# Kernel optimization log

Hardware: AMD Instinct MI355X
Metric: run time of the kernel (lower is better)

## Reference

```python
import jax, jax.numpy as jnp
import numpy as np

L, D, H, V, BS = 12, 768, 12, 50257, 1024  # n_layer, n_embd, n_head, vocab, block_size
B, T = 2, 1024
HD = D // H
SCALE = HD ** -0.5


def setup_inputs() -> dict:
    key = jax.random.key(0)
    ks = jax.random.split(key, 10)
    s = 0.02  # init std from _init_weights
    f = lambda k, shape: jax.random.normal(k, shape, jnp.float32) * s
    return {
        "idx": jax.random.randint(ks[0], (B, T), 0, V),
        "tok_emb": f(ks[1], (V, D)),          # tied with LM head
        "pos_emb": f(ks[2], (BS, D)),
        "wqkv": f(ks[3], (L, 3 * D, D)), "bqkv": jnp.zeros((L, 3 * D), jnp.float32),
        "wproj": f(ks[4], (L, D, D)),    "bproj": jnp.zeros((L, D), jnp.float32),
        "ln1_g": jnp.ones((L, D), jnp.float32), "ln1_b": jnp.zeros((L, D), jnp.float32),
        "ln2_g": jnp.ones((L, D), jnp.float32), "ln2_b": jnp.zeros((L, D), jnp.float32),
        "w1": f(ks[5], (L, 4 * D, D)), "b1": jnp.zeros((L, 4 * D), jnp.float32),
        "w2": f(ks[6], (L, D, 4 * D)), "b2": jnp.zeros((L, D), jnp.float32),
        "lnf_g": jnp.ones((D,), jnp.float32), "lnf_b": jnp.zeros((D,), jnp.float32),
    }


def _ln(x, g, b, eps=1e-5):
    mu = jnp.mean(x, axis=-1, keepdims=True)
    var = jnp.mean(jnp.square(x - mu), axis=-1, keepdims=True)
    return (x - mu) * jax.lax.rsqrt(var + eps) * g + b


def _gpt_forward(idx, tok_emb, pos_emb, wqkv, bqkv, wproj, bproj,
                 ln1_g, ln1_b, ln2_g, ln2_b, w1, b1, w2, b2, lnf_g, lnf_b):
    Bb, Tt = idx.shape
    x = tok_emb[idx] + pos_emb[:Tt]  # [B,T,D]; dropout=0 in eval
    causal = jnp.tril(jnp.ones((Tt, Tt), bool))

    def block(x, p):
        wq, bq, wp, bp, g1, be1, g2, be2, W1, B1, W2, B2 = p
        h = _ln(x, g1, be1)
        qkv = h @ wq.T + bq                       # [B,T,3D]
        q, k, v = jnp.split(qkv, 3, axis=-1)
        to_heads = lambda z: z.reshape(Bb, Tt, H, HD).transpose(0, 2, 1, 3)
        q, k, v = to_heads(q), to_heads(k), to_heads(v)
        att = jnp.einsum('bhqd,bhkd->bhqk', q, k) * SCALE
        att = jnp.where(causal, att, -jnp.inf)
        att = jax.nn.softmax(att, axis=-1)
        y = jnp.einsum('bhqk,bhkd->bhqd', att, v)
        y = y.transpose(0, 2, 1, 3).reshape(Bb, Tt, D)
        x = x + (y @ wp.T + bp)
        h2 = _ln(x, g2, be2)
        ff = jax.nn.gelu(h2 @ W1.T + B1, approximate=False) @ W2.T + B2
        return x + ff, None

    layer_params = (wqkv, bqkv, wproj, bproj, ln1_g, ln1_b, ln2_g, ln2_b, w1, b1, w2, b2)
    x, _ = jax.lax.scan(block, x, layer_params)
    x = _ln(x, lnf_g, lnf_b)
    return x @ tok_emb.T  # tied LM head, [B,T,V]


def reference(idx, tok_emb, pos_emb, wqkv, bqkv, wproj, bproj,
              ln1_g, ln1_b, ln2_g, ln2_b, w1, b1, w2, b2, lnf_g, lnf_b):
    return _gpt_forward(idx, tok_emb, pos_emb, wqkv, bqkv, wproj, bproj,
                        ln1_g, ln1_b, ln2_g, ln2_b, w1, b1, w2, b2, lnf_g, lnf_b)
```

## Files before the change

kernel.cpp:

```cpp
#include <hip/hip_runtime.h>
#include <hip/hip_bf16.h>
#include <type_traits>

#define TT 1024
#define DD 768
#define HH 12
#define LL 12
#define VV 50257
#define MROWS 2048

typedef __attribute__((ext_vector_type(4))) float f32x4;
typedef __attribute__((ext_vector_type(16))) float f32x16;
typedef __attribute__((ext_vector_type(8))) short bf16x8;

__device__ __forceinline__ short f2bf(float f) {
  __hip_bfloat16 h = __float2bfloat16(f);
  short s;
  __builtin_memcpy(&s, &h, 2);
  return s;
}

__device__ __forceinline__ void gload16(const void* g, void* l) {
  __builtin_amdgcn_global_load_lds(
      (const __attribute__((address_space(1))) unsigned int*)g,
      (__attribute__((address_space(3))) unsigned int*)l, 16, 0, 0);
}

__device__ __forceinline__ float wsum(float v) {
#pragma unroll
  for (int o = 32; o; o >>= 1) v += __shfl_xor(v, o, 64);
  return v;
}

struct CvtArgs { const float* s[5]; short* d[5]; long n4[5]; };

__global__ __launch_bounds__(256) void cvt5_k(CvtArgs a, long tot)
{
  const long stride = (long)gridDim.x * 256;
  for (long i = (long)blockIdx.x * 256 + threadIdx.x; i < tot; i += stride) {
    long off = i;
    int s = 0;
#pragma unroll
    for (int q = 0; q < 4; ++q) {
      if (off >= a.n4[s]) { off -= a.n4[s]; ++s; }
    }
    const float4 v = ((const float4*)a.s[s])[off];
    short4 h;
    h.x = f2bf(v.x); h.y = f2bf(v.y); h.z = f2bf(v.z); h.w = f2bf(v.w);
    ((short4*)a.d[s])[off] = h;
  }
}

__global__ __launch_bounds__(256) void embed_k(const int* __restrict__ idx,
    const float* __restrict__ tok, const float* __restrict__ pos,
    float* __restrict__ x)
{
  int i = blockIdx.x * 256 + threadIdx.x;
  int d = i % DD;
  int bt = i / DD;
  int t = bt & (TT - 1);
  x[i] = tok[(long)idx[bt] * DD + d] + pos[t * DD + d];
}

__global__ __launch_bounds__(256) void ln_k(const float* __restrict__ x,
    const float* __restrict__ g, const float* __restrict__ b,
    short* __restrict__ out)
{
  const int w = threadIdx.x >> 6;
  const int lane = threadIdx.x & 63;
  const int row = blockIdx.x * 4 + w;
  const float* xr = x + (long)row * DD;
  float4 v[3];
  float s = 0.f, s2 = 0.f;
#pragma unroll
  for (int i = 0; i < 3; ++i) {
    v[i] = ((const float4*)xr)[lane + i * 64];
    s  += v[i].x + v[i].y + v[i].z + v[i].w;
    s2 += v[i].x * v[i].x + v[i].y * v[i].y + v[i].z * v[i].z + v[i].w * v[i].w;
  }
  s = wsum(s); s2 = wsum(s2);
  const float mu = s * (1.f / DD);
  const float var = s2 * (1.f / DD) - mu * mu;
  const float rstd = rsqrtf(var + 1e-5f);
#pragma unroll
  for (int i = 0; i < 3; ++i) {
    const int d0 = (lane + i * 64) * 4;
    short4 h;
    h.x = f2bf((v[i].x - mu) * rstd * g[d0 + 0] + b[d0 + 0]);
    h.y = f2bf((v[i].y - mu) * rstd * g[d0 + 1] + b[d0 + 1]);
    h.z = f2bf((v[i].z - mu) * rstd * g[d0 + 2] + b[d0 + 2]);
    h.w = f2bf((v[i].w - mu) * rstd * g[d0 + 3] + b[d0 + 3]);
    ((short4*)(out + (long)row * DD))[lane + i * 64] = h;
  }
}

__global__ __launch_bounds__(256) void flash_k(const short* __restrict__ qkv,
                                               const short* __restrict__ vt,
                                               short* __restrict__ y)
{
  const int qt = (int)gridDim.x - 1 - (int)blockIdx.x;
  const int z  = blockIdx.y;
  const int zb = z / HH, zh = z % HH;
  const int w    = threadIdx.x >> 6;
  const int lane = threadIdx.x & 63;
  const int c = lane & 15, g = lane >> 4;

  __shared__ __align__(16) short Pl[4][16][72];
  __shared__ float Ol[4][16][64];
  __shared__ float ml[4][16], ll[4][16];

  const int qbase = qt * 16;
  const long rowQ = (long)(zb * TT + qbase + c) * (3 * DD) + zh * 64;

  bf16x8 qf[2];
  qf[0] = *(const bf16x8*)(qkv + rowQ + g * 8);
  qf[1] = *(const bf16x8*)(qkv + rowQ + 32 + g * 8);

  f32x4 O[4] = {};
  f32x4 mrun, lrun;
#pragma unroll
  for (int r = 0; r < 4; ++r) { mrun[r] = -1e30f; lrun[r] = 0.f; }

  const float CSC = 0.125f * 1.44269504089f;
  const int nt = (qbase + 15) / 64 + 1;

  for (int t = w; t < nt; t += 4) {
    const int k0 = t * 64;
    f32x4 acc[4] = {};
#pragma unroll
    for (int nf = 0; nf < 4; ++nf) {
      const long rowK = (long)(zb * TT + k0 + nf * 16 + c) * (3 * DD) + DD + zh * 64;
      bf16x8 kf0 = *(const bf16x8*)(qkv + rowK + g * 8);
      bf16x8 kf1 = *(const bf16x8*)(qkv + rowK + 32 + g * 8);
      acc[nf] = __builtin_amdgcn_mfma_f32_16x16x32_bf16(qf[0], kf0, acc[nf], 0, 0, 0);
      acc[nf] = __builtin_amdgcn_mfma_f32_16x16x32_bf16(qf[1], kf1, acc[nf], 0, 0, 0);
    }
    f32x4 tv[4];
    const int mask_needed = (k0 + 63 > qbase);
#pragma unroll
    for (int nf = 0; nf < 4; ++nf) {
      const int k_abs = k0 + nf * 16 + c;
#pragma unroll
      for (int r = 0; r < 4; ++r) {
        float val = acc[nf][r] * CSC;
        if (mask_needed && k_abs > qbase + g * 4 + r) val = -1e30f;
        tv[nf][r] = val;
      }
    }
    f32x4 rmax;
#pragma unroll
    for (int r = 0; r < 4; ++r)
      rmax[r] = fmaxf(fmaxf(tv[0][r], tv[1][r]), fmaxf(tv[2][r], tv[3][r]));
#pragma unroll
    for (int off = 1; off < 16; off <<= 1) {
#pragma unroll
      for (int r = 0; r < 4; ++r) rmax[r] = fmaxf(rmax[r], __shfl_xor(rmax[r], off, 64));
    }
    f32x4 mnew, rfac;
#pragma unroll
    for (int r = 0; r < 4; ++r) {
      mnew[r] = fmaxf(mrun[r], rmax[r]);
      rfac[r] = exp2f(mrun[r] - mnew[r]);
      mrun[r] = mnew[r];
    }
    f32x4 e[4], rsum;
#pragma unroll
    for (int r = 0; r < 4; ++r) rsum[r] = 0.f;
#pragma unroll
    for (int nf = 0; nf < 4; ++nf)
#pragma unroll
      for (int r = 0; r < 4; ++r) {
        e[nf][r] = exp2f(tv[nf][r] - mnew[r]);
        rsum[r] += e[nf][r];
      }
#pragma unroll
    for (int off = 1; off < 16; off <<= 1) {
#pragma unroll
      for (int r = 0; r < 4; ++r) rsum[r] += __shfl_xor(rsum[r], off, 64);
    }
#pragma unroll
    for (int r = 0; r < 4; ++r) lrun[r] = lrun[r] * rfac[r] + rsum[r];
#pragma unroll
    for (int nf = 0; nf < 4; ++nf)
#pragma unroll
      for (int r = 0; r < 4; ++r) O[nf][r] *= rfac[r];
#pragma unroll
    for (int nf = 0; nf < 4; ++nf)
#pragma unroll
      for (int r = 0; r < 4; ++r)
        Pl[w][g * 4 + r][nf * 16 + c] = f2bf(e[nf][r]);
    asm volatile("s_waitcnt lgkmcnt(0)" ::: "memory");
    bf16x8 pf[2];
    pf[0] = *(const bf16x8*)&Pl[w][c][g * 8];
    pf[1] = *(const bf16x8*)&Pl[w][c][32 + g * 8];
#pragma unroll
    for (int nf = 0; nf < 4; ++nf) {
      const long vrow = ((long)z * 64 + nf * 16 + c) * TT + k0;
      const bf16x8 vf0 = *(const bf16x8*)(vt + vrow + g * 8);
      const bf16x8 vf1 = *(const bf16x8*)(vt + vrow + 32 + g * 8);
      O[nf] = __builtin_amdgcn_mfma_f32_16x16x32_bf16(pf[0], vf0, O[nf], 0, 0, 0);
      O[nf] = __builtin_amdgcn_mfma_f32_16x16x32_bf16(pf[1], vf1, O[nf], 0, 0, 0);
    }
  }

#pragma unroll
  for (int nf = 0; nf < 4; ++nf)
#pragma unroll
    for (int r = 0; r < 4; ++r)
      Ol[w][g * 4 + r][nf * 16 + c] = O[nf][r];
  if (c == 0) {
#pragma unroll
    for (int r = 0; r < 4; ++r) { ml[w][g * 4 + r] = mrun[r]; ll[w][g * 4 + r] = lrun[r]; }
  }
  __syncthreads();

  for (int e2 = threadIdx.x; e2 < 16 * 64; e2 += 256) {
    const int row = e2 >> 6, d = e2 & 63;
    const float M = fmaxf(fmaxf(ml[0][row], ml[1][row]), fmaxf(ml[2][row], ml[3][row]));
    float L = 0.f, Ov = 0.f;
#pragma unroll
    for (int u = 0; u < 4; ++u) {
      const float f = exp2f(ml[u][row] - M);
      L += ll[u][row] * f;
      Ov += Ol[u][row][d] * f;
    }
    y[(long)(zb * TT + qbase + row) * DD + zh * 64 + d] = f2bf(Ov / L);
  }
}

template<int BM, int BN, int BK, int MFS, typename TB, int EPI, bool LMSWZ, bool PIPE>
__global__ __launch_bounds__(256) void gemm_nt(
    const short* __restrict__ A, const TB* __restrict__ Bm,
    const float* __restrict__ bias, const float* __restrict__ resid,
    void* __restrict__ Cout,
    int M, int N, int K, int lda, int ldb, int ldc,
    long aSB, long aSH, long bSB, long bSH, long cSB, long cSH,
    float scale, int causal)
{
  int n0, m0;
  if constexpr (LMSWZ) {
    const int l = blockIdx.x;
    const int x = l & 7;
    const int j = l >> 3;
    const int mt = j & 15;
    const int nl = j >> 4;
    const int npan = (N + BN - 1) / BN;
    const int q = npan >> 3, rr = npan & 7;
    const int cnt = q + (x < rr);
    if (nl >= cnt) return;
    const int nstart = x * q + (x < rr ? x : rr);
    n0 = (nstart + nl) * BN;
    m0 = mt * BM;
  } else {
    n0 = blockIdx.x * BN;
    m0 = blockIdx.y * BM;
  }
  if (causal && n0 >= m0 + BM) return;
  const int z = blockIdx.z;
  const int zb = z / HH, zh = z % HH;
  const short* Ag = A + zb * aSB + zh * aSH + (long)m0 * lda;
  const TB*    Bg = Bm + zb * bSB + zh * bSH;
  const long  cOff = zb * cSB + zh * cSH;

  constexpr int NBUF = PIPE ? 2 : 1;
  __shared__ __align__(16) short Als[NBUF][BM][BK];
  __shared__ __align__(16) short Bls[NBUF][BN][BK];

  const int tid = threadIdx.x;
  const int lane = tid & 63, wid = tid >> 6;
  constexpr int WTM = BM / 2, WTN = BN / 2;
  constexpr int FM = WTM / 16, FN = WTN / 16;
  constexpr int FM2 = (MFS == 32) ? WTM / 32 : 1;
  constexpr int FN2 = (MFS == 32) ? WTN / 32 : 1;
  constexpr int AM = (MFS == 16) ? FM : FM2;
  constexpr int AN = (MFS == 16) ? FN : FN2;
  const int wr = wid >> 1, wc = wid & 1;

  using accT = typename std::conditional<MFS == 16, f32x4, f32x16>::type;
  accT acc[AM][AN] = {};

  constexpr bool B_IS_F32 = (sizeof(TB) == 4);
  constexpr int CPR = BK / 8;
  constexpr int NCA = BM * CPR;
  constexpr int NCB = BN * CPR;
  constexpr int IA = NCA / 256, IB = NCB / 256;
  constexpr int GPT = IA + IB;
  static_assert(CPR == 8, "swizzle assumes 128B rows (BK=64)");
  static_assert(B_IS_F32 || (NCA % 256 == 0 && NCB % 256 == 0), "chunk grid");

  auto compute = [&](int buf) {
    if constexpr (MFS == 16) {
      const int kAoff = (lane >> 4) * 8;
#pragma unroll
      for (int kk = 0; kk < BK; kk += 32) {
        bf16x8 af[AM], bfr[AN];
#pragma unroll
        for (int mi = 0; mi < AM; ++mi) {
          const int Ra = wr * WTM + mi * 16 + (lane & 15);
          const int kca = (kk + kAoff) >> 3;
          af[mi] = *(const bf16x8*)&Als[buf][Ra][(kca ^ (Ra & 7)) << 3];
        }
#pragma unroll
        for (int ni = 0; ni < AN; ++ni) {
          const int Rb = wc * WTN + ni * 16 + (lane & 15);
          const int kcb = (kk + kAoff) >> 3;
          bfr[ni] = *(const bf16x8*)&Bls[buf][Rb][(kcb ^ (Rb & 7)) << 3];
        }
#pragma unroll
        for (int mi = 0; mi < AM; ++mi)
#pragma unroll
          for (int ni = 0; ni < AN; ++ni)
            acc[mi][ni] = __builtin_amdgcn_mfma_f32_16x16x32_bf16(af[mi], bfr[ni], acc[mi][ni], 0, 0, 0);
      }
    } else {
#pragma unroll
      for (int kk = 0; kk < BK; kk += 16) {
        const int kc = (kk >> 3) + (lane >> 5);
        bf16x8 af[AM], bfr[AN];
#pragma unroll
        for (int mi = 0; mi < AM; ++mi) {
          const int Ra = wr * WTM + mi * 32 + (lane & 31);
          af[mi] = *(const bf16x8*)&Als[buf][Ra][(kc ^ (Ra & 7)) << 3];
        }
#pragma unroll
        for (int ni = 0; ni < AN; ++ni) {
          const int Rb = wc * WTN + ni * 32 + (lane & 31);
          bfr[ni] = *(const bf16x8*)&Bls[buf][Rb][(kc ^ (Rb & 7)) << 3];
        }
#pragma unroll
        for (int mi = 0; mi < AM; ++mi)
#pragma unroll
          for (int ni = 0; ni < AN; ++ni)
            acc[mi][ni] = __builtin_amdgcn_mfma_f32_32x32x16_bf16(af[mi], bfr[ni], acc[mi][ni], 0, 0, 0);
      }
    }
  };

  if constexpr (!B_IS_F32) {
    const short* ap[IA];
    const short* bp[IB];
#pragma unroll
    for (int i = 0; i < IA; ++i) {
      const int cch = i * 256 + tid;
      const int r = cch / CPR, kc = cch % CPR;
      ap[i] = Ag + (long)r * lda + ((kc ^ (r & 7)) << 3);
    }
#pragma unroll
    for (int i = 0; i < IB; ++i) {
      const int cch = i * 256 + tid;
      const int r = cch / CPR, kc = cch % CPR;
      int gr = n0 + r; gr = (gr < N) ? gr : (N - 1);
      bp[i] = (const short*)Bg + (long)gr * ldb + ((kc ^ (r & 7)) << 3);
    }
    const int ldsoff = wid * 64 * 16;

    auto stage = [&](int buf) {
#pragma unroll
      for (int i = 0; i < IA; ++i) {
        gload16(ap[i], (char*)&Als[buf][0][0] + i * 4096 + ldsoff);
        ap[i] += BK;
      }
#pragma unroll
      for (int i = 0; i < IB; ++i) {
        gload16(bp[i], (char*)&Bls[buf][0][0] + i * 4096 + ldsoff);
        bp[i] += BK;
      }
    };

    if constexpr (PIPE) {
      const int KT = K / BK;
      stage(0);
      for (int kt = 0; kt < KT; ++kt) {
        const int cur = kt & 1;
        if (kt + 1 < KT) {
          stage(cur ^ 1);
          asm volatile("s_waitcnt vmcnt(%0)" :: "i"(GPT));
        } else {
          asm volatile("s_waitcnt vmcnt(0)");
        }
        __builtin_amdgcn_sched_barrier(0);
        __builtin_amdgcn_s_barrier();
        __builtin_amdgcn_sched_barrier(0);
        compute(cur);
        asm volatile("" ::: "memory");
        __builtin_amdgcn_s_barrier();
        __builtin_amdgcn_sched_barrier(0);
      }
    } else {
      const int KT = K / BK;
      for (int kt = 0; kt < KT; ++kt) {
        stage(0);
        __syncthreads();
        compute(0);
        __syncthreads();
      }
    }
  } else {
    for (int k0 = 0; k0 < K; k0 += BK) {
#pragma unroll
      for (int cc = tid; cc < BM * (BK / 8); cc += 256) {
        int r = cc / (BK / 8), kc = cc % (BK / 8);
        const uint4 v = *(const uint4*)(Ag + (long)r * lda + k0 + kc * 8);
        *(uint4*)((char*)&Als[0][r][0] + ((kc ^ (r & 7)) << 4)) = v;
      }
#pragma unroll
      for (int cc = tid; cc < BN * (BK / 4); cc += 256) {
        int r = cc / (BK / 4), kc = cc % (BK / 4);
        int gr = n0 + r; gr = (gr < N) ? gr : (N - 1);
        const float4 v = *(const float4*)((const float*)Bg + (long)gr * ldb + k0 + kc * 4);
        short4 h4;
        h4.x = f2bf(v.x); h4.y = f2bf(v.y); h4.z = f2bf(v.z); h4.w = f2bf(v.w);
        *(short4*)((char*)&Bls[0][r][0] + ((kc * 8) ^ ((r & 7) << 4))) = h4;
      }
      __syncthreads();
      compute(0);
      __syncthreads();
    }
  }

  if constexpr (MFS == 16) {
    const int rq = (lane >> 4) << 2;
    const int cl = lane & 15;
#pragma unroll
    for (int mi = 0; mi < AM; ++mi) {
#pragma unroll
      for (int ni = 0; ni < AN; ++ni) {
        const int cg = n0 + wc * WTN + ni * 16 + cl;
        if (cg >= N) continue;
        const int rbase = m0 + wr * WTM + mi * 16 + rq;
        if constexpr (EPI == 5) {
          if (cg >= 2 * DD) {
            const int hh = (cg - 2 * DD) >> 6, dd2 = (cg - 2 * DD) & 63;
            const int bI = rbase >> 10, tI = rbase & (TT - 1);
            const float bv = bias[cg];
            short4 h4;
            h4.x = f2bf(acc[mi][ni][0] + bv);
            h4.y = f2bf(acc[mi][ni][1] + bv);
            h4.z = f2bf(acc[mi][ni][2] + bv);
            h4.w = f2bf(acc[mi][ni][3] + bv);
            short* vtp = (short*)(void*)resid;
            *(short4*)(vtp + (((long)(bI * HH + hh) * 64 + dd2) << 10) + tI) = h4;
          } else {
#pragma unroll
            for (int q = 0; q < 4; ++q)
              ((short*)Cout)[(long)(rbase + q) * ldc + cg] = f2bf(acc[mi][ni][q] + bias[cg]);
          }
          continue;
        }
#pragma unroll
        for (int q = 0; q < 4; ++q) {
          const long cidx = cOff + (long)(rbase + q) * ldc + cg;
          const float v = acc[mi][ni][q];
          if constexpr (EPI == 0) {
            ((float*)Cout)[cidx] = v * scale;
          } else if constexpr (EPI == 1) {
            ((short*)Cout)[cidx] = f2bf(v + bias[cg]);
          } else if constexpr (EPI == 2) {
            ((float*)Cout)[cidx] = resid[cidx] + v + bias[cg];
          } else if constexpr (EPI == 3) {
            const float zz = v + bias[cg];
            ((short*)Cout)[cidx] = f2bf(0.5f * zz * (1.f + erff(zz * 0.70710678118f)));
          } else {
            ((short*)Cout)[cidx] = f2bf(v);
          }
        }
      }
    }
  } else {
    const int cl = lane & 31;
    const int rhi = (lane >> 5) * 4;
#pragma unroll
    for (int mi = 0; mi < AM; ++mi) {
#pragma unroll
      for (int ni = 0; ni < AN; ++ni) {
        const int cg = n0 + wc * WTN + ni * 32 + cl;
        if (cg >= N) continue;
#pragma unroll
        for (int reg = 0; reg < 16; ++reg) {
          const int row = m0 + wr * WTM + mi * 32 + (reg & 3) + ((reg >> 2) * 8) + rhi;
          const long cidx = cOff + (long)row * ldc + cg;
          const float v = acc[mi][ni][reg];
          if constexpr (EPI == 0) {
            ((float*)Cout)[cidx] = v * scale;
          } else if constexpr (EPI == 1) {
            ((short*)Cout)[cidx] = f2bf(v + bias[cg]);
          } else if constexpr (EPI == 2) {
            ((float*)Cout)[cidx] = resid[cidx] + v + bias[cg];
          } else if constexpr (EPI == 3) {
            const float zz = v + bias[cg];
            ((short*)Cout)[cidx] = f2bf(0.5f * zz * (1.f + erff(zz * 0.70710678118f)));
          } else {
            ((short*)Cout)[cidx] = f2bf(v);
          }
        }
      }
    }
  }
}

template<typename TB>
static void run_model(const int* idx, const float* tok_f, const float* pos,
                      const TB* wqkv, const float* bqkv, const TB* wproj, const float* bproj,
                      const float* ln1g, const float* ln1b, const float* ln2g, const float* ln2b,
                      const TB* w1, const float* b1, const TB* w2, const float* b2,
                      const float* lnfg, const float* lnfb, const TB* tok_w,
                      float* xa, float* xb, short* hbf, short* qkv, short* vt,
                      short* ybf, short* ffb,
                      float* out, hipStream_t stream)
{
  embed_k<<<dim3(MROWS * DD / 256), 256, 0, stream>>>(idx, tok_f, pos, xa);

  float* xc = xa;
  float* xn = xb;
  for (int l = 0; l < LL; ++l) {
    ln_k<<<dim3(MROWS / 4), 256, 0, stream>>>(xc, ln1g + l * DD, ln1b + l * DD, hbf);
    gemm_nt<128, 64, 64, 16, TB, 5, false, true><<<dim3(36, 16, 1), 256, 0, stream>>>(
        hbf, wqkv + (long)l * 3 * DD * DD, bqkv + l * 3 * DD, (const float*)vt, qkv,
        MROWS, 3 * DD, DD, DD, DD, 3 * DD, 0, 0, 0, 0, 0, 0, 1.f, 0);
    flash_k<<<dim3(64, 24), 256, 0, stream>>>(qkv, vt, ybf);
    gemm_nt<64, 64, 64, 16, TB, 2, false, true><<<dim3(12, 32, 1), 256, 0, stream>>>(
        ybf, wproj + (long)l * DD * DD, bproj + l * DD, xc, xn,
        MROWS, DD, DD, DD, DD, DD, 0, 0, 0, 0, 0, 0, 1.f, 0);
    ln_k<<<dim3(MROWS / 4), 256, 0, stream>>>(xn, ln2g + l * DD, ln2b + l * DD, hbf);
    gemm_nt<128, 64, 64, 16, TB, 3, false, true><<<dim3(48, 16, 1), 256, 0, stream>>>(
        hbf, w1 + (long)l * 4 * DD * DD, b1 + l * 4 * DD, nullptr, ffb,
        MROWS, 4 * DD, DD, DD, DD, 4 * DD, 0, 0, 0, 0, 0, 0, 1.f, 0);
    gemm_nt<64, 64, 64, 16, TB, 2, false, true><<<dim3(12, 32, 1), 256, 0, stream>>>(
        ffb, w2 + (long)l * DD * 4 * DD, b2 + l * DD, xn, xc,
        MROWS, DD, 4 * DD, 4 * DD, 4 * DD, DD, 0, 0, 0, 0, 0, 0, 1.f, 0);
  }
  ln_k<<<dim3(MROWS / 4), 256, 0, stream>>>(xc, lnfg, lnfb, hbf);
  gemm_nt<128, 128, 64, 32, TB, 0, true, false><<<dim3(6400, 1, 1), 256, 0, stream>>>(
      hbf, tok_w, nullptr, nullptr, out,
      MROWS, VV, DD, DD, DD, VV, 0, 0, 0, 0, 0, 0, 1.f, 0);
}

extern "C" void kernel_launch(void* const* d_in, const int* in_sizes, int n_in,
                              void* d_out, int out_size, void* d_ws, size_t ws_size,
                              hipStream_t stream)
{
  const int*   idx  = (const int*)d_in[0];
  const float* tok  = (const float*)d_in[1];
  const float* pos  = (const float*)d_in[2];
  const float* wqkv = (const float*)d_in[3];
  const float* bqkv = (const float*)d_in[4];
  const float* wproj= (const float*)d_in[5];
  const float* bproj= (const float*)d_in[6];
  const float* ln1g = (const float*)d_in[7];
  const float* ln1b = (const float*)d_in[8];
  const float* ln2g = (const float*)d_in[9];
  const float* ln2b = (const float*)d_in[10];
  const float* w1   = (const float*)d_in[11];
  const float* b1   = (const float*)d_in[12];
  const float* w2   = (const float*)d_in[13];
  const float* b2   = (const float*)d_in[14];
  const float* lnfg = (const float*)d_in[15];
  const float* lnfb = (const float*)d_in[16];
  float* out = (float*)d_out;

  const long E_WQKV = (long)LL * 3 * DD * DD;
  const long E_WPRJ = (long)LL * DD * DD;
  const long E_W1   = (long)LL * 4 * DD * DD;
  const long E_W2   = E_W1;
  const long E_TOK  = (long)VV * DD;
  const long E_WSUM = E_WQKV + E_WPRJ + E_W1 + E_W2 + E_TOK;

  const size_t NEED_B = 44040192;
  const size_t NEED_A = NEED_B + 2 * (size_t)E_WSUM;

  if (ws_size < NEED_B) return;
  const bool bf16w = (ws_size >= NEED_A);

  char* ws = (char*)d_ws;
  short *wqkv_h = nullptr, *wprj_h = nullptr, *w1_h = nullptr, *w2_h = nullptr, *tok_h = nullptr;
  if (bf16w) {
    wqkv_h = (short*)ws; ws += E_WQKV * 2;
    wprj_h = (short*)ws; ws += E_WPRJ * 2;
    w1_h   = (short*)ws; ws += E_W1 * 2;
    w2_h   = (short*)ws; ws += E_W2 * 2;
    tok_h  = (short*)ws; ws += E_TOK * 2;
  }
  float* xa  = (float*)ws; ws += (size_t)MROWS * DD * 4;
  float* xb  = (float*)ws; ws += (size_t)MROWS * DD * 4;
  short* hbf = (short*)ws; ws += (size_t)MROWS * DD * 2;
  short* qkv = (short*)ws; ws += (size_t)MROWS * 3 * DD * 2;
  short* vt  = (short*)ws; ws += (size_t)24 * 64 * TT * 2;
  short* ybf = (short*)ws; ws += (size_t)MROWS * DD * 2;
  short* ffb = (short*)ws; ws += (size_t)MROWS * 4 * DD * 2;

  if (bf16w) {
    CvtArgs ca;
    ca.s[0] = wqkv; ca.d[0] = wqkv_h; ca.n4[0] = E_WQKV / 4;
    ca.s[1] = wproj; ca.d[1] = wprj_h; ca.n4[1] = E_WPRJ / 4;
    ca.s[2] = w1;   ca.d[2] = w1_h;   ca.n4[2] = E_W1 / 4;
    ca.s[3] = w2;   ca.d[3] = w2_h;   ca.n4[3] = E_W2 / 4;
    ca.s[4] = tok;  ca.d[4] = tok_h;  ca.n4[4] = E_TOK / 4;
    const long tot = (E_WQKV + E_WPRJ + E_W1 + E_W2 + E_TOK) / 4;
    cvt5_k<<<dim3(4096), 256, 0, stream>>>(ca, tot);
    run_model<short>(idx, tok, pos, wqkv_h, bqkv, wprj_h, bproj,
                     ln1g, ln1b, ln2g, ln2b, w1_h, b1, w2_h, b2, lnfg, lnfb, tok_h,
                     xa, xb, hbf, qkv, vt, ybf, ffb, out, stream);
  } else {
    run_model<float>(idx, tok, pos, wqkv, bqkv, wproj, bproj,
                     ln1g, ln1b, ln2g, ln2b, w1, b1, w2, b2, lnfg, lnfb, tok,
                     xa, xb, hbf, qkv, vt, ybf, ffb, out, stream);
  }
}
```

Measured before the change: 2.253 ms.

## Interleave A and B tiles in one LDS row for the 32x32 MFMA GEMM path

For the 32x32 MFMA variant, A and B tiles now share one LDS buffer where each row holds the A slice followed by the B slice (256 bytes), with a 16-way XOR swizzle. A single loop of global-to-LDS loads then fills both operands, and the fragment reads go through the wider swizzle. The aim is to change the LDS bank-conflict pattern and the load issue structure. The new path requires BM==BN and no double buffering, so those configurations give up pipelining.

```diff
diff --git a/kernel.cpp b/kernel.cpp
--- a/kernel.cpp
+++ b/kernel.cpp
@@ -263,8 +263,8 @@
   const long  cOff = zb * cSB + zh * cSH;
 
   constexpr int NBUF = PIPE ? 2 : 1;
-  __shared__ __align__(16) short Als[NBUF][BM][BK];
-  __shared__ __align__(16) short Bls[NBUF][BN][BK];
+  static_assert(MFS == 16 || (BM == BN && !PIPE), "ILV path needs BM==BN, single-buffer");
+  __shared__ __align__(16) short LDSb[NBUF * (BM + BN) * BK];
 
   const int tid = threadIdx.x;
   const int lane = tid & 63, wid = tid >> 6;
@@ -285,12 +285,17 @@
   constexpr int NCB = BN * CPR;
   constexpr int IA = NCA / 256, IB = NCB / 256;
   constexpr int GPT = IA + IB;
-  static_assert(CPR == 8, "swizzle assumes 128B rows (BK=64)");
+  static_assert(CPR == 8, "swizzle assumes 128B operand rows (BK=64)");
   static_assert(B_IS_F32 || (NCA % 256 == 0 && NCB % 256 == 0), "chunk grid");
+
+  auto aTile = [&](int buf) -> short* { return LDSb + buf * BM * BK; };
+  auto bTile = [&](int buf) -> short* { return LDSb + NBUF * BM * BK + buf * BN * BK; };
 
   auto compute = [&](int buf) {
     if constexpr (MFS == 16) {
       const int kAoff = (lane >> 4) * 8;
+      short* Als = aTile(buf);
+      short* Bls = bTile(buf);
 #pragma unroll
       for (int kk = 0; kk < BK; kk += 32) {
         bf16x8 af[AM], bfr[AN];
@@ -298,13 +303,13 @@
         for (int mi = 0; mi < AM; ++mi) {
           const int Ra = wr * WTM + mi * 16 + (lane & 15);
           const int kca = (kk + kAoff) >> 3;
-          af[mi] = *(const bf16x8*)&Als[buf][Ra][(kca ^ (Ra & 7)) << 3];
+          af[mi] = *(const bf16x8*)&Als[Ra * BK + ((kca ^ (Ra & 7)) << 3)];
         }
 #pragma unroll
         for (int ni = 0; ni < AN; ++ni) {
           const int Rb = wc * WTN + ni * 16 + (lane & 15);
           const int kcb = (kk + kAoff) >> 3;
-          bfr[ni] = *(const bf16x8*)&Bls[buf][Rb][(kcb ^ (Rb & 7)) << 3];
+          bfr[ni] = *(const bf16x8*)&Bls[Rb * BK + ((kcb ^ (Rb & 7)) << 3)];
         }
 #pragma unroll
         for (int mi = 0; mi < AM; ++mi)
@@ -320,12 +325,12 @@
 #pragma unroll
         for (int mi = 0; mi < AM; ++mi) {
           const int Ra = wr * WTM + mi * 32 + (lane & 31);
-          af[mi] = *(const bf16x8*)&Als[buf][Ra][(kc ^ (Ra & 7)) << 3];
+          af[mi] = *(const bf16x8*)&LDSb[Ra * (2 * BK) + ((kc ^ (Ra & 15)) << 3)];
         }
 #pragma unroll
         for (int ni = 0; ni < AN; ++ni) {
           const int Rb = wc * WTN + ni * 32 + (lane & 31);
-          bfr[ni] = *(const bf16x8*)&Bls[buf][Rb][(kc ^ (Rb & 7)) << 3];
+          bfr[ni] = *(const bf16x8*)&LDSb[Rb * (2 * BK) + (((8 + kc) ^ (Rb & 15)) << 3)];
         }
 #pragma unroll
         for (int mi = 0; mi < AM; ++mi)
@@ -337,80 +342,130 @@
   };
 
   if constexpr (!B_IS_F32) {
-    const short* ap[IA];
-    const short* bp[IB];
-#pragma unroll
-    for (int i = 0; i < IA; ++i) {
-      const int cch = i * 256 + tid;
-      const int r = cch / CPR, kc = cch % CPR;
-      ap[i] = Ag + (long)r * lda + ((kc ^ (r & 7)) << 3);
-    }
-#pragma unroll
-    for (int i = 0; i < IB; ++i) {
-      const int cch = i * 256 + tid;
-      const int r = cch / CPR, kc = cch % CPR;
-      int gr = n0 + r; gr = (gr < N) ? gr : (N - 1);
-      bp[i] = (const short*)Bg + (long)gr * ldb + ((kc ^ (r & 7)) << 3);
-    }
     const int ldsoff = wid * 64 * 16;
-
-    auto stage = [&](int buf) {
-#pragma unroll
-      for (int i = 0; i < IA; ++i) {
-        gload16(ap[i], (char*)&Als[buf][0][0] + i * 4096 + ldsoff);
-        ap[i] += BK;
-      }
-#pragma unroll
-      for (int i = 0; i < IB; ++i) {
-        gload16(bp[i], (char*)&Bls[buf][0][0] + i * 4096 + ldsoff);
-        bp[i] += BK;
-      }
-    };
-
-    if constexpr (PIPE) {
-      const int KT = K / BK;
-      stage(0);
-      for (int kt = 0; kt < KT; ++kt) {
-        const int cur = kt & 1;
-        if (kt + 1 < KT) {
-          stage(cur ^ 1);
-          asm volatile("s_waitcnt vmcnt(%0)" :: "i"(GPT));
+    if constexpr (MFS == 32) {
+      constexpr int IT = BM * 16 / 256;
+      const short* abp[IT];
+#pragma unroll
+      for (int i = 0; i < IT; ++i) {
+        const int cc = i * 256 + tid;
+        const int r = cc >> 4, cl = cc & 15;
+        const int co = cl ^ (r & 15);
+        if (co < 8) {
+          abp[i] = Ag + (long)r * lda + co * 8;
         } else {
-          asm volatile("s_waitcnt vmcnt(0)");
-        }
-        __builtin_amdgcn_sched_barrier(0);
-        __builtin_amdgcn_s_barrier();
-        __builtin_amdgcn_sched_barrier(0);
-        compute(cur);
-        asm volatile("" ::: "memory");
-        __builtin_amdgcn_s_barrier();
-        __builtin_amdgcn_sched_barrier(0);
-      }
-    } else {
+          int gr = n0 + r; gr = (gr < N) ? gr : (N - 1);
+          abp[i] = (const short*)Bg + (long)gr * ldb + (co - 8) * 8;
+        }
+      }
       const int KT = K / BK;
       for (int kt = 0; kt < KT; ++kt) {
-        stage(0);
+#pragma unroll
+        for (int i = 0; i < IT; ++i) {
+          gload16(abp[i], (char*)LDSb + i * 4096 + ldsoff);
+          abp[i] += BK;
+        }
         __syncthreads();
         compute(0);
         __syncthreads();
       }
+    } else {
+      const short* ap[IA];
+      const short* bp[IB];
+#pragma unroll
+      for (int i = 0; i < IA; ++i) {
+        const int cch = i * 256 + tid;
+        const int r = cch / CPR, kc = cch % CPR;
+        ap[i] = Ag + (long)r * lda + ((kc ^ (r & 7)) << 3);
+      }
+#pragma unroll
+      for (int i = 0; i < IB; ++i) {
+        const int cch = i * 256 + tid;
+        const int r = cch / CPR, kc = cch % CPR;
+        int gr = n0 + r; gr = (gr < N) ? gr : (N - 1);
+        bp[i] = (const short*)Bg + (long)gr * ldb + ((kc ^ (r & 7)) << 3);
+      }
+
+      auto stage = [&](int buf) {
+#pragma unroll
+        for (int i = 0; i < IA; ++i) {
+          gload16(ap[i], (char*)aTile(buf) + i * 4096 + ldsoff);
+          ap[i] += BK;
+        }
+#pragma unroll
+        for (int i = 0; i < IB; ++i) {
+          gload16(bp[i], (char*)bTile(buf) + i * 4096 + ldsoff);
+          bp[i] += BK;
+        }
+      };
+
+      if constexpr (PIPE) {
+        const int KT = K / BK;
+        stage(0);
+        for (int kt = 0; kt < KT; ++kt) {
+          const int cur = kt & 1;
+          if (kt + 1 < KT) {
+            stage(cur ^ 1);
+            asm volatile("s_waitcnt vmcnt(%0)" :: "i"(GPT));
+          } else {
+            asm volatile("s_waitcnt vmcnt(0)");
+          }
+          __builtin_amdgcn_sched_barrier(0);
+          __builtin_amdgcn_s_barrier();
+          __builtin_amdgcn_sched_barrier(0);
+          compute(cur);
+          asm volatile("" ::: "memory");
+          __builtin_amdgcn_s_barrier();
+          __builtin_amdgcn_sched_barrier(0);
+        }
+      } else {
+        const int KT = K / BK;
+        for (int kt = 0; kt < KT; ++kt) {
+          stage(0);
+          __syncthreads();
+          compute(0);
+          __syncthreads();
+        }
+      }
     }
   } else {
     for (int k0 = 0; k0 < K; k0 += BK) {
-#pragma unroll
-      for (int cc = tid; cc < BM * (BK / 8); cc += 256) {
-        int r = cc / (BK / 8), kc = cc % (BK / 8);
-        const uint4 v = *(const uint4*)(Ag + (long)r * lda + k0 + kc * 8);
-        *(uint4*)((char*)&Als[0][r][0] + ((kc ^ (r & 7)) << 4)) = v;
-      }
-#pragma unroll
-      for (int cc = tid; cc < BN * (BK / 4); cc += 256) {
-        int r = cc / (BK / 4), kc = cc % (BK / 4);
-        int gr = n0 + r; gr = (gr < N) ? gr : (N - 1);
-        const float4 v = *(const float4*)((const float*)Bg + (long)gr * ldb + k0 + kc * 4);
-        short4 h4;
-        h4.x = f2bf(v.x); h4.y = f2bf(v.y); h4.z = f2bf(v.z); h4.w = f2bf(v.w);
-        *(short4*)((char*)&Bls[0][r][0] + ((kc * 8) ^ ((r & 7) << 4))) = h4;
+      if constexpr (MFS == 32) {
+#pragma unroll
+        for (int cc = tid; cc < BM * CPR; cc += 256) {
+          int r = cc / CPR, kc = cc % CPR;
+          const uint4 v = *(const uint4*)(Ag + (long)r * lda + k0 + kc * 8);
+          *(uint4*)&LDSb[r * (2 * BK) + ((kc ^ (r & 15)) << 3)] = v;
+        }
+#pragma unroll
+        for (int cc = tid; cc < BN * (BK / 4); cc += 256) {
+          int r = cc / (BK / 4), kc4 = cc % (BK / 4);
+          int gr = n0 + r; gr = (gr < N) ? gr : (N - 1);
+          const float4 v = *(const float4*)((const float*)Bg + (long)gr * ldb + k0 + kc4 * 4);
+          short4 h4;
+          h4.x = f2bf(v.x); h4.y = f2bf(v.y); h4.z = f2bf(v.z); h4.w = f2bf(v.w);
+          const int co = 8 + (kc4 >> 1);
+          *(short4*)&LDSb[r * (2 * BK) + ((co ^ (r & 15)) << 3) + (kc4 & 1) * 4] = h4;
+        }
+      } else {
+        short* Als = aTile(0);
+        short* Bls = bTile(0);
+#pragma unroll
+        for (int cc = tid; cc < BM * CPR; cc += 256) {
+          int r = cc / CPR, kc = cc % CPR;
+          const uint4 v = *(const uint4*)(Ag + (long)r * lda + k0 + kc * 8);
+          *(uint4*)&Als[r * BK + ((kc ^ (r & 7)) << 3)] = v;
+        }
+#pragma unroll
+        for (int cc = tid; cc < BN * (BK / 4); cc += 256) {
+          int r = cc / (BK / 4), kc4 = cc % (BK / 4);
+          int gr = n0 + r; gr = (gr < N) ? gr : (N - 1);
+          const float4 v = *(const float4*)((const float*)Bg + (long)gr * ldb + k0 + kc4 * 4);
+          short4 h4;
+          h4.x = f2bf(v.x); h4.y = f2bf(v.y); h4.z = f2bf(v.z); h4.w = f2bf(v.w);
+          const int co = kc4 >> 1;
+          *(short4*)&Bls[r * BK + ((co ^ (r & 7)) << 3) + (kc4 & 1) * 4] = h4;
+        }
       }
       __syncthreads();
       compute(0);
```

Result: faster. 2.019 ms, median of 3 (-10.4%).
